# Kernel tuning notes

Measured on AMD Instinct MI355X. Metric: run time of the kernel, lower is better.

The kernel has to match this reference:

```python
import jax, jax.numpy as jnp
import numpy as np

B, S, D, H = 4, 2048, 1024, 16
HD = D // H

def setup_inputs() -> dict:
    key = jax.random.key(0)
    ks = jax.random.split(key, 9)
    s = 1.0 / np.sqrt(D)
    return {
        "x": jax.random.normal(ks[0], (B, S, D), dtype=jnp.float32),
        "wq": jax.random.uniform(ks[1], (D, D), jnp.float32, -s, s),
        "bq": jnp.zeros((D,), jnp.float32),
        "wk": jax.random.uniform(ks[2], (D, D), jnp.float32, -s, s),
        "bk": jnp.zeros((D,), jnp.float32),
        "wv": jax.random.uniform(ks[3], (D, D), jnp.float32, -s, s),
        "bv": jnp.zeros((D,), jnp.float32),
        "wo": jax.random.uniform(ks[4], (D, D), jnp.float32, -s, s),
        "bo": jnp.zeros((D,), jnp.float32),
    }

def reference(x, wq, bq, wk, bk, wv, bv, wo, bo):
    b, s, _ = x.shape
    # project and split heads: [B,S,D] -> [B,H,S,HD]
    def heads(w, bias):
        return (x @ w.T + bias).reshape(b, s, H, HD).transpose(0, 2, 1, 3)
    q = heads(wq, bq)
    k = heads(wk, bk)
    v = heads(wv, bv)
    scale = 1.0 / jnp.sqrt(jnp.float32(HD))
    scores = jnp.einsum("bhqd,bhkd->bhqk", q, k) * scale
    attn = jax.nn.softmax(scores, axis=-1)
    out = jnp.einsum("bhqk,bhkd->bhqd", attn, v)
    out = out.transpose(0, 2, 1, 3).reshape(b, s, D)
    return out @ wo.T + bo
```

## Files before the change

kernel.cpp:

```cpp
#include <hip/hip_runtime.h>
#include <stdint.h>


#define B_ 4
#define S_ 2048
#define D_ 1024
#define H_ 16
#define HD_ 64
#define M_ (B_ * S_)

typedef __bf16 bf16x8 __attribute__((ext_vector_type(8)));
typedef float f32x4 __attribute__((ext_vector_type(4)));
typedef float f32x16 __attribute__((ext_vector_type(16)));
typedef unsigned short u16;
typedef union { bf16x8 v; unsigned u[4]; } bfu;

#define QSCALE 0.18033688011112042f
#define THR2 11.0f

__device__ __forceinline__ u16 f2bf(float f) {
  union { float f; unsigned u; } v; v.f = f;
  unsigned u = v.u;
  u += 0x7fff + ((u >> 16) & 1);
  return (u16)(u >> 16);
}

__device__ __forceinline__ float exp2_fast(float x) {
#if __has_builtin(__builtin_amdgcn_exp2f)
  return __builtin_amdgcn_exp2f(x);
#else
  return __expf(x * 0.69314718056f);
#endif
}

__device__ __forceinline__ unsigned packbf(float a, float b) {
  union { unsigned u; __bf16 h[2]; } v;
  v.h[0] = (__bf16)a; v.h[1] = (__bf16)b;
  return v.u;
}

__device__ __forceinline__ void gl2lds16(const void* g, void* l) {
  __builtin_amdgcn_global_load_lds(
      (const __attribute__((address_space(1))) unsigned int*)g,
      (__attribute__((address_space(3))) unsigned int*)l, 16, 0, 0);
}

__global__ __launch_bounds__(256) void convert_kernel(
    const float* __restrict__ x, const float* __restrict__ wq,
    const float* __restrict__ wk, const float* __restrict__ wv,
    const float* __restrict__ wo, u16* __restrict__ xb, u16* __restrict__ wqb,
    u16* __restrict__ wkb, u16* __restrict__ wvb, u16* __restrict__ wob) {
  const int64_t NX = (int64_t)M_ * D_ / 4;
  const int64_t NW = (int64_t)D_ * D_ / 4;
  int64_t i = (int64_t)blockIdx.x * blockDim.x + threadIdx.x;
  const float* src; u16* dst; int64_t off;
  if (i < NX)              { src = x;  dst = xb;  off = i; }
  else if (i < NX + NW)    { src = wq; dst = wqb; off = i - NX; }
  else if (i < NX + 2*NW)  { src = wk; dst = wkb; off = i - NX - NW; }
  else if (i < NX + 3*NW)  { src = wv; dst = wvb; off = i - NX - 2*NW; }
  else                     { src = wo; dst = wob; off = i - NX - 3*NW; }
  float4 v = reinterpret_cast<const float4*>(src)[off];
  ushort4 o;
  o.x = f2bf(v.x); o.y = f2bf(v.y); o.z = f2bf(v.z); o.w = f2bf(v.w);
  reinterpret_cast<ushort4*>(dst)[off] = o;
}

template <int MODE>
__global__ __launch_bounds__(256) void gemm_kernel(
    const u16* __restrict__ A, const u16* __restrict__ Bw,
    const float* __restrict__ bias, void* __restrict__ out) {
  __shared__ u16 As[128 * 64];
  __shared__ u16 Bs[128 * 64];
  const int tid = threadIdx.x;
  const int lane = tid & 63;
  const int wid = tid >> 6;
  const int row0 = blockIdx.y * 128;
  const int col0 = blockIdx.x * 128;
  const int wr = (wid >> 1) * 64;
  const int wc = (wid & 1) * 64;

  f32x4 acc[4][4] = {};
  const int srow = lane >> 3;
  const int cc = (lane & 7) ^ srow;

  for (int kt = 0; kt < D_; kt += 64) {
    __syncthreads();
    for (int t = 0; t < 4; ++t) {
      int r = (wid * 4 + t) * 8 + srow;
      gl2lds16(A + (int64_t)(row0 + r) * D_ + kt + cc * 8,
               (char*)As + (wid * 4 + t) * 1024);
      gl2lds16(Bw + (int64_t)(col0 + r) * D_ + kt + cc * 8,
               (char*)Bs + (wid * 4 + t) * 1024);
    }
    __syncthreads();

    bf16x8 af[4][2], bfr[4][2];
#pragma unroll
    for (int mi = 0; mi < 4; ++mi)
#pragma unroll
      for (int ks = 0; ks < 2; ++ks) {
        int c = ks * 4 + (lane >> 4);
        int ra = wr + mi * 16 + (lane & 15);
        af[mi][ks] = *reinterpret_cast<const bf16x8*>(
            (char*)As + ra * 128 + ((c ^ (ra & 7)) << 4));
        int rb = wc + mi * 16 + (lane & 15);
        bfr[mi][ks] = *reinterpret_cast<const bf16x8*>(
            (char*)Bs + rb * 128 + ((c ^ (rb & 7)) << 4));
      }
#pragma unroll
    for (int ks = 0; ks < 2; ++ks)
#pragma unroll
      for (int mi = 0; mi < 4; ++mi)
#pragma unroll
        for (int ni = 0; ni < 4; ++ni) {
          if (MODE == 1)
            acc[mi][ni] = __builtin_amdgcn_mfma_f32_16x16x32_bf16(
                bfr[ni][ks], af[mi][ks], acc[mi][ni], 0, 0, 0);
          else
            acc[mi][ni] = __builtin_amdgcn_mfma_f32_16x16x32_bf16(
                af[mi][ks], bfr[ni][ks], acc[mi][ni], 0, 0, 0);
        }
  }

  if (MODE == 0 || MODE == 3) {
    u16* o = (u16*)out;
#pragma unroll
    for (int mi = 0; mi < 4; ++mi)
#pragma unroll
      for (int ni = 0; ni < 4; ++ni) {
        int j = col0 + wc + ni * 16 + (lane & 15);
        float bvv = bias[j];
        int h = j >> 6, hd = j & 63;
#pragma unroll
        for (int r = 0; r < 4; ++r) {
          int i = row0 + wr + mi * 16 + (lane >> 4) * 4 + r;
          int b = i >> 11, s = i & 2047;
          float val = acc[mi][ni][r] + bvv;
          if (MODE == 3) val *= QSCALE;
          o[((int64_t)(b * H_ + h) * S_ + s) * HD_ + hd] = f2bf(val);
        }
      }
  } else if (MODE == 1) {
    u16* o = (u16*)out;
#pragma unroll
    for (int mi = 0; mi < 4; ++mi)
#pragma unroll
      for (int ni = 0; ni < 4; ++ni) {
        int i = row0 + wr + mi * 16 + (lane & 15);
        int b = i >> 11, s = i & 2047;
#pragma unroll
        for (int r = 0; r < 4; ++r) {
          int j = col0 + wc + ni * 16 + (lane >> 4) * 4 + r;
          int h = j >> 6, hd = j & 63;
          o[((int64_t)(b * H_ + h) * HD_ + hd) * S_ + s] = f2bf(acc[mi][ni][r] + bias[j]);
        }
      }
  } else {
    float* o = (float*)out;
#pragma unroll
    for (int mi = 0; mi < 4; ++mi)
#pragma unroll
      for (int ni = 0; ni < 4; ++ni) {
        int j = col0 + wc + ni * 16 + (lane & 15);
        float bvv = bias[j];
#pragma unroll
        for (int r = 0; r < 4; ++r) {
          int i = row0 + wr + mi * 16 + (lane >> 4) * 4 + r;
          o[(int64_t)i * D_ + j] = acc[mi][ni][r] + bvv;
        }
      }
  }
}

__global__ __launch_bounds__(256, 2) void attn_kernel(
    const u16* __restrict__ Q, const u16* __restrict__ Kg,
    const u16* __restrict__ Vt, u16* __restrict__ AO) {
  __shared__ u16 Ks[2][64 * 64];
  __shared__ u16 Vs[2][64 * 64];
  const int tid = threadIdx.x;
  const int lane = tid & 63;
  const int l31 = lane & 31;
  const int hi = lane >> 5;
  const int wid = tid >> 6;
  const int orig = blockIdx.x;
  const int swz = (orig & 7) * 64 + (orig >> 3);
  const int bh = swz >> 3;
  const int qw = (swz & 7) * 256 + wid * 64;

  bf16x8 qf[2][4];
#pragma unroll
  for (int qb = 0; qb < 2; ++qb)
#pragma unroll
    for (int ks = 0; ks < 4; ++ks)
      qf[qb][ks] = *reinterpret_cast<const bf16x8*>(
          Q + ((int64_t)bh * S_ + qw + qb * 32 + l31) * HD_ + ks * 16 + hi * 8);

  bf16x8 ones8;
#pragma unroll
  for (int i = 0; i < 8; ++i) ones8[i] = (__bf16)1.0f;

  f32x16 o0[2] = {}, o1[2] = {}, ls[2] = {};
  float mrow[2] = {-1e30f, -1e30f};

  const int srow = lane >> 3;
  const int cc = (lane & 7) ^ srow;

  const int lr0 = (wid * 2 + 0) * 8 + srow;
  const int lr1 = (wid * 2 + 1) * 8 + srow;
  const int sr0 = (lr0 & ~12) | ((lr0 & 4) << 1) | ((lr0 & 8) >> 1);
  const int sr1 = (lr1 & ~12) | ((lr1 & 4) << 1) | ((lr1 & 8) >> 1);
  const u16* kp0 = Kg + ((int64_t)bh * S_ + sr0) * HD_ + cc * 8;
  const u16* kp1 = Kg + ((int64_t)bh * S_ + sr1) * HD_ + cc * 8;
  const u16* vp0 = Vt + ((int64_t)bh * HD_ + lr0) * S_ + cc * 8;
  const u16* vp1 = Vt + ((int64_t)bh * HD_ + lr1) * S_ + cc * 8;

  gl2lds16(kp0, (char*)Ks[0] + (wid * 2 + 0) * 1024); kp0 += 64 * HD_;
  gl2lds16(kp1, (char*)Ks[0] + (wid * 2 + 1) * 1024); kp1 += 64 * HD_;
  gl2lds16(vp0, (char*)Vs[0] + (wid * 2 + 0) * 1024); vp0 += 64;
  gl2lds16(vp1, (char*)Vs[0] + (wid * 2 + 1) * 1024); vp1 += 64;

  const int NT = S_ / 64;

#define TILE_STEP(T, CUR)                                                      \
  {                                                                            \
    asm volatile("s_waitcnt vmcnt(0)" ::: "memory");                           \
    __builtin_amdgcn_s_barrier();                                              \
    if ((T) + 1 < NT) {                                                        \
      gl2lds16(kp0, (char*)Ks[(CUR) ^ 1] + (wid * 2 + 0) * 1024);              \
      gl2lds16(kp1, (char*)Ks[(CUR) ^ 1] + (wid * 2 + 1) * 1024);              \
      gl2lds16(vp0, (char*)Vs[(CUR) ^ 1] + (wid * 2 + 0) * 1024);              \
      gl2lds16(vp1, (char*)Vs[(CUR) ^ 1] + (wid * 2 + 1) * 1024);              \
      kp0 += 64 * HD_; kp1 += 64 * HD_; vp0 += 64; vp1 += 64;                  \
    }                                                                          \
    f32x16 sc0[2] = {{}, {}}, sc1[2] = {{}, {}};                               \
    {                                                                          \
      const char* kbase = (const char*)Ks[CUR];                                \
      __builtin_amdgcn_s_setprio(1);                                           \
      _Pragma("unroll")                                                        \
      for (int ks = 0; ks < 4; ++ks) {                                         \
        int chunk = 2 * ks + hi;                                               \
        int r0 = l31, r1 = 32 + l31;                                           \
        bf16x8 k0 = *reinterpret_cast<const bf16x8*>(                          \
            kbase + r0 * 128 + ((chunk ^ (r0 & 7)) << 4));                     \
        bf16x8 k1 = *reinterpret_cast<const bf16x8*>(                          \
            kbase + r1 * 128 + ((chunk ^ (r1 & 7)) << 4));                     \
        _Pragma("unroll")                                                      \
        for (int qb = 0; qb < 2; ++qb) {                                       \
          sc0[qb] = __builtin_amdgcn_mfma_f32_32x32x16_bf16(k0, qf[qb][ks],    \
                                                            sc0[qb], 0, 0, 0); \
          sc1[qb] = __builtin_amdgcn_mfma_f32_32x32x16_bf16(k1, qf[qb][ks],    \
                                                            sc1[qb], 0, 0, 0); \
        }                                                                      \
      }                                                                        \
      __builtin_amdgcn_s_setprio(0);                                           \
    }                                                                          \
    float mx[2];                                                               \
    _Pragma("unroll")                                                          \
    for (int qb = 0; qb < 2; ++qb) {                                           \
      float a8[8];                                                             \
      _Pragma("unroll")                                                        \
      for (int i = 0; i < 8; ++i)                                              \
        a8[i] = fmaxf(fmaxf(fmaxf(sc0[qb][2 * i], sc0[qb][2 * i + 1]),         \
                            sc1[qb][2 * i]), sc1[qb][2 * i + 1]);              \
      mx[qb] = fmaxf(fmaxf(fmaxf(fmaxf(a8[0], a8[1]), a8[2]), a8[3]),          \
                     fmaxf(fmaxf(fmaxf(a8[4], a8[5]), a8[6]), a8[7]));         \
    }                                                                          \
    int okd = (mx[0] - mrow[0] <= THR2 && mx[1] - mrow[1] <= THR2) ? 1 : 0;    \
    if (!__all(okd)) {                                                         \
      _Pragma("unroll")                                                        \
      for (int qb = 0; qb < 2; ++qb) {                                         \
        float mxf = fmaxf(mx[qb], __shfl_xor(mx[qb], 32));                     \
        float mnew = fmaxf(mrow[qb], mxf);                                     \
        float al = exp2_fast(mrow[qb] - mnew);                                 \
        mrow[qb] = mnew;                                                       \
        _Pragma("unroll")                                                      \
        for (int tt = 0; tt < 16; ++tt) {                                      \
          float at = __shfl(al, (tt & 3) + 8 * (tt >> 2) + 4 * hi);            \
          o0[qb][tt] *= at; o1[qb][tt] *= at; ls[qb][tt] *= at;                \
        }                                                                      \
      }                                                                        \
    }                                                                          \
    bfu pa[2][4];                                                              \
    _Pragma("unroll")                                                          \
    for (int qb = 0; qb < 2; ++qb) {                                           \
      _Pragma("unroll")                                                        \
      for (int tt = 0; tt < 16; ++tt) {                                        \
        sc0[qb][tt] = exp2_fast(sc0[qb][tt] - mrow[qb]);                       \
        sc1[qb][tt] = exp2_fast(sc1[qb][tt] - mrow[qb]);                       \
      }                                                                        \
      _Pragma("unroll")                                                        \
      for (int m = 0; m < 4; ++m) {                                            \
        pa[qb][0].u[m] = packbf(sc0[qb][2 * m], sc0[qb][2 * m + 1]);           \
        pa[qb][1].u[m] = packbf(sc0[qb][8 + 2 * m], sc0[qb][9 + 2 * m]);       \
        pa[qb][2].u[m] = packbf(sc1[qb][2 * m], sc1[qb][2 * m + 1]);           \
        pa[qb][3].u[m] = packbf(sc1[qb][8 + 2 * m], sc1[qb][9 + 2 * m]);       \
      }                                                                        \
    }                                                                          \
    {                                                                          \
      const char* vbase = (const char*)Vs[CUR];                                \
      __builtin_amdgcn_s_setprio(1);                                           \
      _Pragma("unroll")                                                        \
      for (int kb = 0; kb < 4; ++kb) {                                         \
        int chunk = 2 * kb + hi;                                               \
        int r0 = l31, r1 = 32 + l31;                                           \
        bf16x8 v0 = *reinterpret_cast<const bf16x8*>(                          \
            vbase + r0 * 128 + ((chunk ^ (r0 & 7)) << 4));                     \
        bf16x8 v1 = *reinterpret_cast<const bf16x8*>(                          \
            vbase + r1 * 128 + ((chunk ^ (r1 & 7)) << 4));                     \
        _Pragma("unroll")                                                      \
        for (int qb = 0; qb < 2; ++qb) {                                       \
          o0[qb] = __builtin_amdgcn_mfma_f32_32x32x16_bf16(pa[qb][kb].v, v0,   \
                                                           o0[qb], 0, 0, 0);   \
          o1[qb] = __builtin_amdgcn_mfma_f32_32x32x16_bf16(pa[qb][kb].v, v1,   \
                                                           o1[qb], 0, 0, 0);   \
          ls[qb] = __builtin_amdgcn_mfma_f32_32x32x16_bf16(pa[qb][kb].v,       \
                                                           ones8, ls[qb],      \
                                                           0, 0, 0);           \
        }                                                                      \
      }                                                                        \
      __builtin_amdgcn_s_setprio(0);                                           \
    }                                                                          \
  }

  for (int t = 0; t < NT; t += 2) {
    TILE_STEP(t, 0)
    TILE_STEP(t + 1, 1)
  }
#undef TILE_STEP

  const int b = bh >> 4, h = bh & 15;
#pragma unroll
  for (int qb = 0; qb < 2; ++qb)
#pragma unroll
    for (int tt = 0; tt < 16; ++tt) {
      int row = (tt & 3) + 8 * (tt >> 2) + 4 * hi;
      float inv = __builtin_amdgcn_rcpf(ls[qb][tt]);
      int qr = qw + qb * 32 + row;
      int64_t base = ((int64_t)(b * S_ + qr)) * D_ + h * HD_ + l31;
      AO[base] = f2bf(o0[qb][tt] * inv);
      AO[base + 32] = f2bf(o1[qb][tt] * inv);
    }
}

extern "C" void kernel_launch(void* const* d_in, const int* in_sizes, int n_in,
                              void* d_out, int out_size, void* d_ws, size_t ws_size,
                              hipStream_t stream) {
  const float* x  = (const float*)d_in[0];
  const float* wq = (const float*)d_in[1];
  const float* bq = (const float*)d_in[2];
  const float* wk = (const float*)d_in[3];
  const float* bk = (const float*)d_in[4];
  const float* wv = (const float*)d_in[5];
  const float* bv = (const float*)d_in[6];
  const float* wo = (const float*)d_in[7];
  const float* bo = (const float*)d_in[8];
  char* ws = (char*)d_ws;
  u16* xb  = (u16*)ws;
  u16* wqb = (u16*)(ws + (16ll << 20));
  u16* wkb = (u16*)(ws + (18ll << 20));
  u16* wvb = (u16*)(ws + (20ll << 20));
  u16* wob = (u16*)(ws + (22ll << 20));
  u16* q   = (u16*)(ws + (24ll << 20));
  u16* k   = (u16*)(ws + (40ll << 20));
  u16* vt  = (u16*)(ws + (56ll << 20));
  u16* ao  = xb;

  convert_kernel<<<12288, 256, 0, stream>>>(x, wq, wk, wv, wo, xb, wqb, wkb, wvb, wob);
  dim3 gg(D_ / 128, M_ / 128);
  gemm_kernel<3><<<gg, 256, 0, stream>>>(xb, wqb, bq, q);
  gemm_kernel<0><<<gg, 256, 0, stream>>>(xb, wkb, bk, k);
  gemm_kernel<1><<<gg, 256, 0, stream>>>(xb, wvb, bv, vt);
  attn_kernel<<<512, 256, 0, stream>>>(q, k, vt, ao);
  gemm_kernel<2><<<gg, 256, 0, stream>>>(ao, wob, bo, (float*)d_out);
}
```

Before: 222.7 us.

## Double-buffer GEMM LDS tiles to overlap global loads with MFMA compute

The projection GEMM kernel now keeps two LDS buffers for the A and B tiles. While the MFMAs run on the current k-tile, it issues the global-to-LDS copies for the next one. Each k-step ends with a single vmcnt wait and barrier instead of two __syncthreads around a blocking load, so global memory latency is hidden behind compute. In exchange, LDS use per block doubles to 64KB, which may lower occupancy, and ordering now relies on the manual waitcnt and barrier placement.

Measured after the change: 225.4 us. Within noise of the previous version (+1.2%).

```diff
diff --git a/kernel.cpp b/kernel.cpp
--- a/kernel.cpp
+++ b/kernel.cpp
@@ -69,8 +69,8 @@
 __global__ __launch_bounds__(256) void gemm_kernel(
     const u16* __restrict__ A, const u16* __restrict__ Bw,
     const float* __restrict__ bias, void* __restrict__ out) {
-  __shared__ u16 As[128 * 64];
-  __shared__ u16 Bs[128 * 64];
+  __shared__ u16 As[2][128 * 64];
+  __shared__ u16 Bs[2][128 * 64];
   const int tid = threadIdx.x;
   const int lane = tid & 63;
   const int wid = tid >> 6;
@@ -83,44 +83,71 @@
   const int srow = lane >> 3;
   const int cc = (lane & 7) ^ srow;
 
-  for (int kt = 0; kt < D_; kt += 64) {
-    __syncthreads();
-    for (int t = 0; t < 4; ++t) {
-      int r = (wid * 4 + t) * 8 + srow;
-      gl2lds16(A + (int64_t)(row0 + r) * D_ + kt + cc * 8,
-               (char*)As + (wid * 4 + t) * 1024);
-      gl2lds16(Bw + (int64_t)(col0 + r) * D_ + kt + cc * 8,
-               (char*)Bs + (wid * 4 + t) * 1024);
-    }
-    __syncthreads();
-
-    bf16x8 af[4][2], bfr[4][2];
-#pragma unroll
-    for (int mi = 0; mi < 4; ++mi)
-#pragma unroll
-      for (int ks = 0; ks < 2; ++ks) {
-        int c = ks * 4 + (lane >> 4);
-        int ra = wr + mi * 16 + (lane & 15);
-        af[mi][ks] = *reinterpret_cast<const bf16x8*>(
-            (char*)As + ra * 128 + ((c ^ (ra & 7)) << 4));
-        int rb = wc + mi * 16 + (lane & 15);
-        bfr[mi][ks] = *reinterpret_cast<const bf16x8*>(
-            (char*)Bs + rb * 128 + ((c ^ (rb & 7)) << 4));
-      }
-#pragma unroll
-    for (int ks = 0; ks < 2; ++ks)
-#pragma unroll
-      for (int mi = 0; mi < 4; ++mi)
-#pragma unroll
-        for (int ni = 0; ni < 4; ++ni) {
-          if (MODE == 1)
-            acc[mi][ni] = __builtin_amdgcn_mfma_f32_16x16x32_bf16(
-                bfr[ni][ks], af[mi][ks], acc[mi][ni], 0, 0, 0);
-          else
-            acc[mi][ni] = __builtin_amdgcn_mfma_f32_16x16x32_bf16(
-                af[mi][ks], bfr[ni][ks], acc[mi][ni], 0, 0, 0);
-        }
-  }
+  const u16* ap[4];
+  const u16* bp[4];
+#pragma unroll
+  for (int t = 0; t < 4; ++t) {
+    int r = (wid * 4 + t) * 8 + srow;
+    ap[t] = A + (int64_t)(row0 + r) * D_ + cc * 8;
+    bp[t] = Bw + (int64_t)(col0 + r) * D_ + cc * 8;
+  }
+#pragma unroll
+  for (int t = 0; t < 4; ++t) {
+    gl2lds16(ap[t], (char*)As[0] + (wid * 4 + t) * 1024); ap[t] += 64;
+    gl2lds16(bp[t], (char*)Bs[0] + (wid * 4 + t) * 1024); bp[t] += 64;
+  }
+
+  const int NK = D_ / 64;
+
+#define GSTEP(KT, CUR)                                                         \
+  {                                                                            \
+    asm volatile("s_waitcnt vmcnt(0)" ::: "memory");                           \
+    __builtin_amdgcn_s_barrier();                                              \
+    if ((KT) + 1 < NK) {                                                       \
+      _Pragma("unroll")                                                        \
+      for (int t = 0; t < 4; ++t) {                                            \
+        gl2lds16(ap[t], (char*)As[(CUR) ^ 1] + (wid * 4 + t) * 1024);          \
+        ap[t] += 64;                                                           \
+        gl2lds16(bp[t], (char*)Bs[(CUR) ^ 1] + (wid * 4 + t) * 1024);          \
+        bp[t] += 64;                                                           \
+      }                                                                        \
+    }                                                                          \
+    bf16x8 af[4][2], bfr[4][2];                                                \
+    _Pragma("unroll")                                                          \
+    for (int mi = 0; mi < 4; ++mi) {                                           \
+      _Pragma("unroll")                                                        \
+      for (int ks = 0; ks < 2; ++ks) {                                         \
+        int c = ks * 4 + (lane >> 4);                                          \
+        int ra = wr + mi * 16 + (lane & 15);                                   \
+        af[mi][ks] = *reinterpret_cast<const bf16x8*>(                         \
+            (char*)As[CUR] + ra * 128 + ((c ^ (ra & 7)) << 4));                \
+        int rb = wc + mi * 16 + (lane & 15);                                   \
+        bfr[mi][ks] = *reinterpret_cast<const bf16x8*>(                        \
+            (char*)Bs[CUR] + rb * 128 + ((c ^ (rb & 7)) << 4));                \
+      }                                                                        \
+    }                                                                          \
+    _Pragma("unroll")                                                          \
+    for (int ks = 0; ks < 2; ++ks) {                                           \
+      _Pragma("unroll")                                                        \
+      for (int mi = 0; mi < 4; ++mi) {                                         \
+        _Pragma("unroll")                                                      \
+        for (int ni = 0; ni < 4; ++ni) {                                       \
+          if (MODE == 1)                                                       \
+            acc[mi][ni] = __builtin_amdgcn_mfma_f32_16x16x32_bf16(             \
+                bfr[ni][ks], af[mi][ks], acc[mi][ni], 0, 0, 0);                \
+          else                                                                 \
+            acc[mi][ni] = __builtin_amdgcn_mfma_f32_16x16x32_bf16(             \
+                af[mi][ks], bfr[ni][ks], acc[mi][ni], 0, 0, 0);                \
+        }                                                                      \
+      }                                                                        \
+    }                                                                          \
+  }
+
+  for (int kt2 = 0; kt2 < NK; kt2 += 2) {
+    GSTEP(kt2, 0)
+    GSTEP(kt2 + 1, 1)
+  }
+#undef GSTEP
 
   if (MODE == 0 || MODE == 3) {
     u16* o = (u16*)out;
```
